# Optimization experiments

Hardware: AMD Instinct MI355X
Metric: run time of the kernel (lower is better)

The kernel has to match this reference:

```python
import jax, jax.numpy as jnp
import numpy as np

D_IN = 768
D_OUT = 768
SEQ = 4096


def setup_inputs() -> dict:
    key = jax.random.key(0)
    kx, kq, kk, kv = jax.random.split(key, 4)
    # nn.Linear weight shape is [d_out, d_in]; kaiming-uniform-ish scale
    s = 1.0 / np.sqrt(D_IN)
    return {
        "x": jax.random.normal(kx, (SEQ, D_IN), dtype=jnp.float32),
        "Wq": jax.random.uniform(kq, (D_OUT, D_IN), jnp.float32, -s, s),
        "Wk": jax.random.uniform(kk, (D_OUT, D_IN), jnp.float32, -s, s),
        "Wv": jax.random.uniform(kv, (D_OUT, D_IN), jnp.float32, -s, s),
    }


def reference(x, Wq, Wk, Wv):
    # queries/keys/values: [S, d_out] = x @ W.T
    q = x @ Wq.T
    k = x @ Wk.T
    v = x @ Wv.T
    scale = 1.0 / jnp.sqrt(jnp.asarray(k.shape[-1], x.dtype))
    scores = (q @ k.T) * scale               # [S, S]
    attn = jax.nn.softmax(scores, axis=-1)   # [S, S]
    return attn @ v                          # [S, d_out]
```

## Files before the change

### kernel.cpp

```cpp
#include <hip/hip_runtime.h>
#include <hip/hip_bf16.h>

using bf16 = __hip_bfloat16;
typedef __attribute__((ext_vector_type(4))) float f32x4;
typedef __attribute__((ext_vector_type(8))) short short8;

#define SEQ 4096
#define DIM 768


__global__ void convert_all_kernel(const float* __restrict__ x,
                                   const float* __restrict__ wq,
                                   const float* __restrict__ wk,
                                   const float* __restrict__ wv,
                                   bf16* __restrict__ xc, bf16* __restrict__ wqc,
                                   bf16* __restrict__ wkc, bf16* __restrict__ wvc,
                                   float* __restrict__ denom) {
  const int XB = (SEQ * DIM) / 2048;
  const int WB = (DIM * DIM) / 2048;
  int b = blockIdx.x;
  if (b == 0) {
    float4 z = {0.f, 0.f, 0.f, 0.f};
#pragma unroll
    for (int q = 0; q < 4; q++)
      *(float4*)(denom + (threadIdx.x * 4 + q * 1024)) = z;
  }
  const float* src; bf16* dst; int off;
  if (b < XB)               { src = x;  dst = xc;  off = b * 2048; }
  else if (b < XB + WB)     { src = wq; dst = wqc; off = (b - XB) * 2048; }
  else if (b < XB + 2 * WB) { src = wk; dst = wkc; off = (b - XB - WB) * 2048; }
  else                      { src = wv; dst = wvc; off = (b - XB - 2 * WB) * 2048; }
  int i = off + threadIdx.x * 8;
  float4 f0 = *(const float4*)(src + i);
  float4 f1 = *(const float4*)(src + i + 4);
  bf16 tmp[8];
  tmp[0] = __float2bfloat16(f0.x); tmp[1] = __float2bfloat16(f0.y);
  tmp[2] = __float2bfloat16(f0.z); tmp[3] = __float2bfloat16(f0.w);
  tmp[4] = __float2bfloat16(f1.x); tmp[5] = __float2bfloat16(f1.y);
  tmp[6] = __float2bfloat16(f1.z); tmp[7] = __float2bfloat16(f1.w);
  *(uint4*)(dst + i) = *(const uint4*)tmp;
}

__device__ __forceinline__ void gload_lds16(const bf16* g, bf16* l) {
  __builtin_amdgcn_global_load_lds(
      (const __attribute__((address_space(1))) void*)g,
      (__attribute__((address_space(3))) void*)l,
      16, 0, 0);
}

__device__ __forceinline__ void stage64(const bf16* g, int ldk, bf16* l,
                                        int wave, int lane) {
  int r = lane >> 2;
  int c = (lane & 3) * 8;
  const bf16* gw = g + (size_t)(wave * 32) * ldk;
  bf16* lw = l + wave * 1024;
#pragma unroll
  for (int h = 0; h < 2; h++)
#pragma unroll
    for (int s = 0; s < 2; s++)
      gload_lds16(gw + (size_t)(s * 16 + r) * ldk + h * 32 + c,
                  lw + h * 4096 + s * 512);
}

__device__ __forceinline__ void gemm_core(const bf16* __restrict__ A,
                                          const bf16* __restrict__ B,
                                          int ldk, int klen, int m0, int n0,
                                          f32x4 acc[4][4],
                                          bf16* lA, bf16* lB) {
  const int tid  = threadIdx.x;
  const int wave = tid >> 6, lane = tid & 63;
  const int wm = (wave & 1) * 64, wn = (wave >> 1) * 64;
  const int g = lane >> 4, lr = lane & 15;
  const bf16* Abase = A + (size_t)m0 * ldk;
  const bf16* Bbase = B + (size_t)n0 * ldk;
  for (int kk = 0; kk < klen; kk += 64) {
    stage64(Abase + kk, ldk, lA, wave, lane);
    stage64(Bbase + kk, ldk, lB, wave, lane);
    __syncthreads();
#pragma unroll
    for (int h = 0; h < 2; h++) {
      short8 af[4], bfr[4];
#pragma unroll
      for (int i = 0; i < 4; i++)
        af[i] = *(const short8*)&lA[h * 4096 + (wm + i * 16 + lr) * 32 + g * 8];
#pragma unroll
      for (int j = 0; j < 4; j++)
        bfr[j] = *(const short8*)&lB[h * 4096 + (wn + j * 16 + lr) * 32 + g * 8];
#pragma unroll
      for (int i = 0; i < 4; i++)
#pragma unroll
        for (int j = 0; j < 4; j++)
          acc[i][j] = __builtin_amdgcn_mfma_f32_16x16x32_bf16(af[i], bfr[j], acc[i][j], 0, 0, 0);
    }
    __syncthreads();
  }
}


__global__ __launch_bounds__(256, 3) void qkv_kernel(
    const bf16* __restrict__ x, const bf16* __restrict__ Wq,
    const bf16* __restrict__ Wk, const bf16* __restrict__ Wv,
    bf16* __restrict__ Q, bf16* __restrict__ Kb, bf16* __restrict__ Vt) {
  __shared__ __align__(16) bf16 smem[16384];
  bf16* lA = smem;
  bf16* lB = smem + 8192;
  const int m0  = blockIdx.x * 128;
  const int n0g = blockIdx.y * 128;
  const int wsel = n0g / DIM;
  const int n0   = n0g % DIM;
  const bf16* W = (wsel == 0) ? Wq : (wsel == 1) ? Wk : Wv;
  f32x4 acc[4][4] = {};
  gemm_core(x, W, DIM, DIM, m0, n0, acc, lA, lB);

  const int tid = threadIdx.x, wave = tid >> 6, lane = tid & 63;
  const int wm = (wave & 1) * 64, wn = (wave >> 1) * 64;
  const int g = lane >> 4, lr = lane & 15;
  const float scale = 0.03608439182435161f;

  if (wsel == 2) {
    bf16* tile = smem;
#pragma unroll
    for (int ph = 0; ph < 2; ph++) {
      __syncthreads();
      if ((wave >> 1) == ph) {
#pragma unroll
        for (int i = 0; i < 4; i++)
#pragma unroll
          for (int j = 0; j < 4; j++)
#pragma unroll
            for (int r = 0; r < 4; r++)
              tile[(wm + i * 16 + g * 4 + r) * 67 + j * 16 + lr] =
                  __float2bfloat16(acc[i][j][r]);
      }
      __syncthreads();
      int cl = tid >> 2;
      int r0 = (tid & 3) * 32;
      bf16 vals[32];
#pragma unroll
      for (int k = 0; k < 32; k++) vals[k] = tile[(r0 + k) * 67 + cl];
      bf16* dst = Vt + (size_t)(n0 + ph * 64 + cl) * SEQ + m0 + r0;
#pragma unroll
      for (int q = 0; q < 4; q++)
        *(uint4*)(dst + q * 8) = *(const uint4*)(vals + q * 8);
    }
  } else {
    bf16* dstm = (wsel == 0) ? Q : Kb;
    float fs = (wsel == 0) ? scale : 1.0f;
#pragma unroll
    for (int i = 0; i < 4; i++)
#pragma unroll
      for (int j = 0; j < 4; j++)
#pragma unroll
        for (int r = 0; r < 4; r++) {
          int row = m0 + wm + i * 16 + g * 4 + r;
          int col = n0 + wn + j * 16 + lr;
          dstm[row * DIM + col] = __float2bfloat16(acc[i][j][r] * fs);
        }
  }
}

__global__ __launch_bounds__(256, 3) void score_kernel(
    const bf16* __restrict__ Q, const bf16* __restrict__ Kb,
    bf16* __restrict__ P, float* __restrict__ denom) {
  __shared__ __align__(16) bf16 smem[16384];
  bf16* lA = smem;
  bf16* lB = smem + 8192;
  const int m0 = blockIdx.x * 128;
  const int n0 = blockIdx.y * 128;
  f32x4 acc[4][4] = {};
  gemm_core(Q, Kb, DIM, DIM, m0, n0, acc, lA, lB);

  const int tid = threadIdx.x, wave = tid >> 6, lane = tid & 63;
  const int wm = (wave & 1) * 64, wn = (wave >> 1) * 64;
  const int g = lane >> 4, lr = lane & 15;
#pragma unroll
  for (int i = 0; i < 4; i++) {
    float rsum[4] = {0.f, 0.f, 0.f, 0.f};
#pragma unroll
    for (int j = 0; j < 4; j++)
#pragma unroll
      for (int r = 0; r < 4; r++) {
        float p = __expf(acc[i][j][r]);
        int row = m0 + wm + i * 16 + g * 4 + r;
        int col = n0 + wn + j * 16 + lr;
        P[row * SEQ + col] = __float2bfloat16(p);
        rsum[r] += p;
      }
#pragma unroll
    for (int r = 0; r < 4; r++) {
      float s = rsum[r];
      s += __shfl_xor(s, 1);
      s += __shfl_xor(s, 2);
      s += __shfl_xor(s, 4);
      s += __shfl_xor(s, 8);
      if (lr == 0) atomicAdd(&denom[m0 + wm + i * 16 + g * 4 + r], s);
    }
  }
}

__global__ __launch_bounds__(256, 3) void pv_kernel(
    const bf16* __restrict__ P, const bf16* __restrict__ Vt,
    bf16* __restrict__ partial) {
  __shared__ __align__(16) bf16 smem[16384];
  bf16* lA = smem;
  bf16* lB = smem + 8192;
  const int m0 = blockIdx.x * 128;
  const int n0 = blockIdx.y * 128;
  const int kbase = blockIdx.z * (SEQ / 4);
  f32x4 acc[4][4] = {};
  gemm_core(P + kbase, Vt + kbase, SEQ, SEQ / 4, m0, n0, acc, lA, lB);

  bf16* pout = partial + (size_t)blockIdx.z * SEQ * DIM;
  const int tid = threadIdx.x, wave = tid >> 6, lane = tid & 63;
  const int wm = (wave & 1) * 64, wn = (wave >> 1) * 64;
  const int g = lane >> 4, lr = lane & 15;
#pragma unroll
  for (int i = 0; i < 4; i++)
#pragma unroll
    for (int j = 0; j < 4; j++)
#pragma unroll
      for (int r = 0; r < 4; r++) {
        int row = m0 + wm + i * 16 + g * 4 + r;
        int col = n0 + wn + j * 16 + lr;
        pout[row * DIM + col] = __float2bfloat16(acc[i][j][r]);
      }
}

__global__ __launch_bounds__(256) void reduce_kernel(
    const bf16* __restrict__ partial, const float* __restrict__ denom,
    float* __restrict__ out) {
  const size_t stride = (size_t)SEQ * DIM;
  int i = (blockIdx.x * 256 + threadIdx.x) * 8;
  uint4 u0 = *(const uint4*)(partial + i);
  uint4 u1 = *(const uint4*)(partial + stride + i);
  uint4 u2 = *(const uint4*)(partial + 2 * stride + i);
  uint4 u3 = *(const uint4*)(partial + 3 * stride + i);
  bf16 a0[8], a1[8], a2[8], a3[8];
  *(uint4*)a0 = u0; *(uint4*)a1 = u1; *(uint4*)a2 = u2; *(uint4*)a3 = u3;
  float inv = 1.0f / denom[i / DIM];
  float o[8];
#pragma unroll
  for (int k = 0; k < 8; k++)
    o[k] = (__bfloat162float(a0[k]) + __bfloat162float(a1[k]) +
            __bfloat162float(a2[k]) + __bfloat162float(a3[k])) * inv;
  *(float4*)(out + i)     = *(const float4*)(o);
  *(float4*)(out + i + 4) = *(const float4*)(o + 4);
}

extern "C" void kernel_launch(void* const* d_in, const int* in_sizes, int n_in,
                              void* d_out, int out_size, void* d_ws, size_t ws_size,
                              hipStream_t stream) {
  const float* x_raw  = (const float*)d_in[0];
  const float* Wq_raw = (const float*)d_in[1];
  const float* Wk_raw = (const float*)d_in[2];
  const float* Wv_raw = (const float*)d_in[3];
  float* out = (float*)d_out;

  bf16* xc  = (bf16*)d_ws;
  bf16* Wqc = xc  + (size_t)SEQ * DIM;
  bf16* Wkc = Wqc + (size_t)DIM * DIM;
  bf16* Wvc = Wkc + (size_t)DIM * DIM;
  bf16* Q   = Wvc + (size_t)DIM * DIM;
  bf16* Kb  = Q   + (size_t)SEQ * DIM;
  bf16* Vt  = Kb  + (size_t)SEQ * DIM;
  bf16* P   = Vt  + (size_t)DIM * SEQ;
  float* denom  = (float*)(P + (size_t)SEQ * SEQ);
  bf16* partial = (bf16*)(denom + SEQ);

  const int nx = SEQ * DIM;
  const int nw = DIM * DIM;
  const int conv_blocks = nx / 2048 + 3 * (nw / 2048);

  convert_all_kernel<<<conv_blocks, 256, 0, stream>>>(
      x_raw, Wq_raw, Wk_raw, Wv_raw, xc, Wqc, Wkc, Wvc, denom);
  qkv_kernel<<<dim3(SEQ / 128, 2304 / 128), 256, 0, stream>>>(xc, Wqc, Wkc, Wvc, Q, Kb, Vt);
  score_kernel<<<dim3(SEQ / 128, SEQ / 128), 256, 0, stream>>>(Q, Kb, P, denom);
  pv_kernel<<<dim3(SEQ / 128, DIM / 128, 4), 256, 0, stream>>>(P, Vt, partial);
  reduce_kernel<<<nx / 8 / 256, 256, 0, stream>>>(partial, denom, out);
}
```

Baseline: 167.1 us.

## Load GEMM fragments directly from global memory with padded row strides

```diff
diff --git a/kernel.cpp b/kernel.cpp
--- a/kernel.cpp
+++ b/kernel.cpp
@@ -7,6 +7,8 @@
 
 #define SEQ 4096
 #define DIM 768
+#define LDQ 800
+#define LDP 4128
 
 
 __global__ void convert_all_kernel(const float* __restrict__ x,
@@ -16,101 +18,73 @@
                                    bf16* __restrict__ xc, bf16* __restrict__ wqc,
                                    bf16* __restrict__ wkc, bf16* __restrict__ wvc,
                                    float* __restrict__ denom) {
-  const int XB = (SEQ * DIM) / 2048;
-  const int WB = (DIM * DIM) / 2048;
+  const int XB = SEQ * 96 / 256;
+  const int WB = DIM * 96 / 256;
   int b = blockIdx.x;
   if (b == 0) {
     float4 z = {0.f, 0.f, 0.f, 0.f};
 #pragma unroll
     for (int q = 0; q < 4; q++)
-      *(float4*)(denom + (threadIdx.x * 4 + q * 1024)) = z;
-  }
-  const float* src; bf16* dst; int off;
-  if (b < XB)               { src = x;  dst = xc;  off = b * 2048; }
-  else if (b < XB + WB)     { src = wq; dst = wqc; off = (b - XB) * 2048; }
-  else if (b < XB + 2 * WB) { src = wk; dst = wkc; off = (b - XB - WB) * 2048; }
-  else                      { src = wv; dst = wvc; off = (b - XB - 2 * WB) * 2048; }
-  int i = off + threadIdx.x * 8;
-  float4 f0 = *(const float4*)(src + i);
-  float4 f1 = *(const float4*)(src + i + 4);
+      *(float4*)(denom + threadIdx.x * 4 + q * 1024) = z;
+  }
+  const float* src; bf16* dst; int t;
+  if (b < XB)               { src = x;  dst = xc;  t = b * 256 + threadIdx.x; }
+  else if (b < XB + WB)     { src = wq; dst = wqc; t = (b - XB) * 256 + threadIdx.x; }
+  else if (b < XB + 2 * WB) { src = wk; dst = wkc; t = (b - XB - WB) * 256 + threadIdx.x; }
+  else                      { src = wv; dst = wvc; t = (b - XB - 2 * WB) * 256 + threadIdx.x; }
+  int row = t / 96;
+  int col = (t - row * 96) * 8;
+  const float* s = src + row * DIM + col;
+  float4 f0 = *(const float4*)s;
+  float4 f1 = *(const float4*)(s + 4);
   bf16 tmp[8];
   tmp[0] = __float2bfloat16(f0.x); tmp[1] = __float2bfloat16(f0.y);
   tmp[2] = __float2bfloat16(f0.z); tmp[3] = __float2bfloat16(f0.w);
   tmp[4] = __float2bfloat16(f1.x); tmp[5] = __float2bfloat16(f1.y);
   tmp[6] = __float2bfloat16(f1.z); tmp[7] = __float2bfloat16(f1.w);
-  *(uint4*)(dst + i) = *(const uint4*)tmp;
-}
-
-__device__ __forceinline__ void gload_lds16(const bf16* g, bf16* l) {
-  __builtin_amdgcn_global_load_lds(
-      (const __attribute__((address_space(1))) void*)g,
-      (__attribute__((address_space(3))) void*)l,
-      16, 0, 0);
-}
-
-__device__ __forceinline__ void stage64(const bf16* g, int ldk, bf16* l,
-                                        int wave, int lane) {
-  int r = lane >> 2;
-  int c = (lane & 3) * 8;
-  const bf16* gw = g + (size_t)(wave * 32) * ldk;
-  bf16* lw = l + wave * 1024;
-#pragma unroll
-  for (int h = 0; h < 2; h++)
-#pragma unroll
-    for (int s = 0; s < 2; s++)
-      gload_lds16(gw + (size_t)(s * 16 + r) * ldk + h * 32 + c,
-                  lw + h * 4096 + s * 512);
-}
-
-__device__ __forceinline__ void gemm_core(const bf16* __restrict__ A,
-                                          const bf16* __restrict__ B,
-                                          int ldk, int klen, int m0, int n0,
-                                          f32x4 acc[4][4],
-                                          bf16* lA, bf16* lB) {
-  const int tid  = threadIdx.x;
+  *(uint4*)(dst + row * LDQ + col) = *(const uint4*)tmp;
+}
+
+__device__ __forceinline__ void gemm_direct(const bf16* __restrict__ A,
+                                            const bf16* __restrict__ B,
+                                            int ldk, int klen, int m0, int n0,
+                                            f32x4 acc[4][4]) {
+  const int tid = threadIdx.x;
   const int wave = tid >> 6, lane = tid & 63;
   const int wm = (wave & 1) * 64, wn = (wave >> 1) * 64;
   const int g = lane >> 4, lr = lane & 15;
-  const bf16* Abase = A + (size_t)m0 * ldk;
-  const bf16* Bbase = B + (size_t)n0 * ldk;
-  for (int kk = 0; kk < klen; kk += 64) {
-    stage64(Abase + kk, ldk, lA, wave, lane);
-    stage64(Bbase + kk, ldk, lB, wave, lane);
-    __syncthreads();
-#pragma unroll
-    for (int h = 0; h < 2; h++) {
-      short8 af[4], bfr[4];
-#pragma unroll
-      for (int i = 0; i < 4; i++)
-        af[i] = *(const short8*)&lA[h * 4096 + (wm + i * 16 + lr) * 32 + g * 8];
+  const bf16* Ab = A + (size_t)(m0 + wm + lr) * ldk + g * 8;
+  const bf16* Bb = B + (size_t)(n0 + wn + lr) * ldk + g * 8;
+  const size_t r16 = (size_t)16 * ldk;
+  for (int kk = 0; kk < klen; kk += 32) {
+    short8 af[4], bfr[4];
+#pragma unroll
+    for (int i = 0; i < 4; i++)
+      af[i] = *(const short8*)(Ab + i * r16 + kk);
+#pragma unroll
+    for (int j = 0; j < 4; j++)
+      bfr[j] = *(const short8*)(Bb + j * r16 + kk);
+#pragma unroll
+    for (int i = 0; i < 4; i++)
 #pragma unroll
       for (int j = 0; j < 4; j++)
-        bfr[j] = *(const short8*)&lB[h * 4096 + (wn + j * 16 + lr) * 32 + g * 8];
-#pragma unroll
-      for (int i = 0; i < 4; i++)
-#pragma unroll
-        for (int j = 0; j < 4; j++)
-          acc[i][j] = __builtin_amdgcn_mfma_f32_16x16x32_bf16(af[i], bfr[j], acc[i][j], 0, 0, 0);
-    }
-    __syncthreads();
-  }
-}
-
-
-__global__ __launch_bounds__(256, 3) void qkv_kernel(
+        acc[i][j] = __builtin_amdgcn_mfma_f32_16x16x32_bf16(af[i], bfr[j], acc[i][j], 0, 0, 0);
+  }
+}
+
+
+__global__ __launch_bounds__(256, 4) void qkv_kernel(
     const bf16* __restrict__ x, const bf16* __restrict__ Wq,
     const bf16* __restrict__ Wk, const bf16* __restrict__ Wv,
     bf16* __restrict__ Q, bf16* __restrict__ Kb, bf16* __restrict__ Vt) {
-  __shared__ __align__(16) bf16 smem[16384];
-  bf16* lA = smem;
-  bf16* lB = smem + 8192;
+  __shared__ __align__(16) bf16 tile[128 * 67];
   const int m0  = blockIdx.x * 128;
   const int n0g = blockIdx.y * 128;
   const int wsel = n0g / DIM;
   const int n0   = n0g % DIM;
   const bf16* W = (wsel == 0) ? Wq : (wsel == 1) ? Wk : Wv;
   f32x4 acc[4][4] = {};
-  gemm_core(x, W, DIM, DIM, m0, n0, acc, lA, lB);
+  gemm_direct(x, W, LDQ, DIM, m0, n0, acc);
 
   const int tid = threadIdx.x, wave = tid >> 6, lane = tid & 63;
   const int wm = (wave & 1) * 64, wn = (wave >> 1) * 64;
@@ -118,7 +92,6 @@
   const float scale = 0.03608439182435161f;
 
   if (wsel == 2) {
-    bf16* tile = smem;
 #pragma unroll
     for (int ph = 0; ph < 2; ph++) {
       __syncthreads();
@@ -138,7 +111,7 @@
       bf16 vals[32];
 #pragma unroll
       for (int k = 0; k < 32; k++) vals[k] = tile[(r0 + k) * 67 + cl];
-      bf16* dst = Vt + (size_t)(n0 + ph * 64 + cl) * SEQ + m0 + r0;
+      bf16* dst = Vt + (size_t)(n0 + ph * 64 + cl) * LDP + m0 + r0;
 #pragma unroll
       for (int q = 0; q < 4; q++)
         *(uint4*)(dst + q * 8) = *(const uint4*)(vals + q * 8);
@@ -154,21 +127,18 @@
         for (int r = 0; r < 4; r++) {
           int row = m0 + wm + i * 16 + g * 4 + r;
           int col = n0 + wn + j * 16 + lr;
-          dstm[row * DIM + col] = __float2bfloat16(acc[i][j][r] * fs);
+          dstm[row * LDQ + col] = __float2bfloat16(acc[i][j][r] * fs);
         }
   }
 }
 
-__global__ __launch_bounds__(256, 3) void score_kernel(
+__global__ __launch_bounds__(256, 4) void score_kernel(
     const bf16* __restrict__ Q, const bf16* __restrict__ Kb,
     bf16* __restrict__ P, float* __restrict__ denom) {
-  __shared__ __align__(16) bf16 smem[16384];
-  bf16* lA = smem;
-  bf16* lB = smem + 8192;
   const int m0 = blockIdx.x * 128;
   const int n0 = blockIdx.y * 128;
   f32x4 acc[4][4] = {};
-  gemm_core(Q, Kb, DIM, DIM, m0, n0, acc, lA, lB);
+  gemm_direct(Q, Kb, LDQ, DIM, m0, n0, acc);
 
   const int tid = threadIdx.x, wave = tid >> 6, lane = tid & 63;
   const int wm = (wave & 1) * 64, wn = (wave >> 1) * 64;
@@ -183,7 +153,7 @@
         float p = __expf(acc[i][j][r]);
         int row = m0 + wm + i * 16 + g * 4 + r;
         int col = n0 + wn + j * 16 + lr;
-        P[row * SEQ + col] = __float2bfloat16(p);
+        P[(size_t)row * LDP + col] = __float2bfloat16(p);
         rsum[r] += p;
       }
 #pragma unroll
@@ -198,17 +168,14 @@
   }
 }
 
-__global__ __launch_bounds__(256, 3) void pv_kernel(
+__global__ __launch_bounds__(256, 4) void pv_kernel(
     const bf16* __restrict__ P, const bf16* __restrict__ Vt,
     bf16* __restrict__ partial) {
-  __shared__ __align__(16) bf16 smem[16384];
-  bf16* lA = smem;
-  bf16* lB = smem + 8192;
   const int m0 = blockIdx.x * 128;
   const int n0 = blockIdx.y * 128;
   const int kbase = blockIdx.z * (SEQ / 4);
   f32x4 acc[4][4] = {};
-  gemm_core(P + kbase, Vt + kbase, SEQ, SEQ / 4, m0, n0, acc, lA, lB);
+  gemm_direct(P + kbase, Vt + kbase, LDP, SEQ / 4, m0, n0, acc);
 
   bf16* pout = partial + (size_t)blockIdx.z * SEQ * DIM;
   const int tid = threadIdx.x, wave = tid >> 6, lane = tid & 63;
@@ -257,24 +224,22 @@
   float* out = (float*)d_out;
 
   bf16* xc  = (bf16*)d_ws;
-  bf16* Wqc = xc  + (size_t)SEQ * DIM;
-  bf16* Wkc = Wqc + (size_t)DIM * DIM;
-  bf16* Wvc = Wkc + (size_t)DIM * DIM;
-  bf16* Q   = Wvc + (size_t)DIM * DIM;
-  bf16* Kb  = Q   + (size_t)SEQ * DIM;
-  bf16* Vt  = Kb  + (size_t)SEQ * DIM;
-  bf16* P   = Vt  + (size_t)DIM * SEQ;
-  float* denom  = (float*)(P + (size_t)SEQ * SEQ);
+  bf16* Wqc = xc  + (size_t)SEQ * LDQ;
+  bf16* Wkc = Wqc + (size_t)DIM * LDQ;
+  bf16* Wvc = Wkc + (size_t)DIM * LDQ;
+  bf16* Q   = Wvc + (size_t)DIM * LDQ;
+  bf16* Kb  = Q   + (size_t)SEQ * LDQ;
+  bf16* Vt  = Kb  + (size_t)SEQ * LDQ;
+  bf16* P   = Vt  + (size_t)DIM * LDP;
+  float* denom  = (float*)(P + (size_t)SEQ * LDP);
   bf16* partial = (bf16*)(denom + SEQ);
 
-  const int nx = SEQ * DIM;
-  const int nw = DIM * DIM;
-  const int conv_blocks = nx / 2048 + 3 * (nw / 2048);
+  const int conv_blocks = SEQ * 96 / 256 + 3 * (DIM * 96 / 256);
 
   convert_all_kernel<<<conv_blocks, 256, 0, stream>>>(
       x_raw, Wq_raw, Wk_raw, Wv_raw, xc, Wqc, Wkc, Wvc, denom);
   qkv_kernel<<<dim3(SEQ / 128, 2304 / 128), 256, 0, stream>>>(xc, Wqc, Wkc, Wvc, Q, Kb, Vt);
   score_kernel<<<dim3(SEQ / 128, SEQ / 128), 256, 0, stream>>>(Q, Kb, P, denom);
   pv_kernel<<<dim3(SEQ / 128, DIM / 128, 4), 256, 0, stream>>>(P, Vt, partial);
-  reduce_kernel<<<nx / 8 / 256, 256, 0, stream>>>(partial, denom, out);
-}
+  reduce_kernel<<<SEQ * DIM / 8 / 256, 256, 0, stream>>>(partial, denom, out);
+}
```

Measured after the change: 251.6 us. 50.5% more time.

## Fuse split-K reduction and normalization into PV kernel via atomic adds

Applied to the files above, without the earlier changes.

```diff
diff --git a/kernel.cpp b/kernel.cpp
--- a/kernel.cpp
+++ b/kernel.cpp
@@ -15,7 +15,8 @@
                                    const float* __restrict__ wv,
                                    bf16* __restrict__ xc, bf16* __restrict__ wqc,
                                    bf16* __restrict__ wkc, bf16* __restrict__ wvc,
-                                   float* __restrict__ denom) {
+                                   float* __restrict__ denom,
+                                   float* __restrict__ out) {
   const int XB = (SEQ * DIM) / 2048;
   const int WB = (DIM * DIM) / 2048;
   int b = blockIdx.x;
@@ -23,10 +24,15 @@
     float4 z = {0.f, 0.f, 0.f, 0.f};
 #pragma unroll
     for (int q = 0; q < 4; q++)
-      *(float4*)(denom + (threadIdx.x * 4 + q * 1024)) = z;
+      *(float4*)(denom + threadIdx.x * 4 + q * 1024) = z;
   }
   const float* src; bf16* dst; int off;
-  if (b < XB)               { src = x;  dst = xc;  off = b * 2048; }
+  if (b < XB) {
+    src = x; dst = xc; off = b * 2048;
+    float4 z = {0.f, 0.f, 0.f, 0.f};
+    float* o = out + off + threadIdx.x * 8;
+    *(float4*)o = z; *(float4*)(o + 4) = z;
+  }
   else if (b < XB + WB)     { src = wq; dst = wqc; off = (b - XB) * 2048; }
   else if (b < XB + 2 * WB) { src = wk; dst = wkc; off = (b - XB - WB) * 2048; }
   else                      { src = wv; dst = wvc; off = (b - XB - 2 * WB) * 2048; }
@@ -183,7 +189,7 @@
         float p = __expf(acc[i][j][r]);
         int row = m0 + wm + i * 16 + g * 4 + r;
         int col = n0 + wn + j * 16 + lr;
-        P[row * SEQ + col] = __float2bfloat16(p);
+        P[(size_t)row * SEQ + col] = __float2bfloat16(p);
         rsum[r] += p;
       }
 #pragma unroll
@@ -200,7 +206,7 @@
 
 __global__ __launch_bounds__(256, 3) void pv_kernel(
     const bf16* __restrict__ P, const bf16* __restrict__ Vt,
-    bf16* __restrict__ partial) {
+    const float* __restrict__ denom, float* __restrict__ out) {
   __shared__ __align__(16) bf16 smem[16384];
   bf16* lA = smem;
   bf16* lB = smem + 8192;
@@ -210,41 +216,24 @@
   f32x4 acc[4][4] = {};
   gemm_core(P + kbase, Vt + kbase, SEQ, SEQ / 4, m0, n0, acc, lA, lB);
 
-  bf16* pout = partial + (size_t)blockIdx.z * SEQ * DIM;
   const int tid = threadIdx.x, wave = tid >> 6, lane = tid & 63;
   const int wm = (wave & 1) * 64, wn = (wave >> 1) * 64;
   const int g = lane >> 4, lr = lane & 15;
 #pragma unroll
-  for (int i = 0; i < 4; i++)
+  for (int i = 0; i < 4; i++) {
+    float inv[4];
+#pragma unroll
+    for (int r = 0; r < 4; r++)
+      inv[r] = 1.0f / denom[m0 + wm + i * 16 + g * 4 + r];
 #pragma unroll
     for (int j = 0; j < 4; j++)
 #pragma unroll
       for (int r = 0; r < 4; r++) {
         int row = m0 + wm + i * 16 + g * 4 + r;
         int col = n0 + wn + j * 16 + lr;
-        pout[row * DIM + col] = __float2bfloat16(acc[i][j][r]);
+        atomicAdd(&out[row * DIM + col], acc[i][j][r] * inv[r]);
       }
-}
-
-__global__ __launch_bounds__(256) void reduce_kernel(
-    const bf16* __restrict__ partial, const float* __restrict__ denom,
-    float* __restrict__ out) {
-  const size_t stride = (size_t)SEQ * DIM;
-  int i = (blockIdx.x * 256 + threadIdx.x) * 8;
-  uint4 u0 = *(const uint4*)(partial + i);
-  uint4 u1 = *(const uint4*)(partial + stride + i);
-  uint4 u2 = *(const uint4*)(partial + 2 * stride + i);
-  uint4 u3 = *(const uint4*)(partial + 3 * stride + i);
-  bf16 a0[8], a1[8], a2[8], a3[8];
-  *(uint4*)a0 = u0; *(uint4*)a1 = u1; *(uint4*)a2 = u2; *(uint4*)a3 = u3;
-  float inv = 1.0f / denom[i / DIM];
-  float o[8];
-#pragma unroll
-  for (int k = 0; k < 8; k++)
-    o[k] = (__bfloat162float(a0[k]) + __bfloat162float(a1[k]) +
-            __bfloat162float(a2[k]) + __bfloat162float(a3[k])) * inv;
-  *(float4*)(out + i)     = *(const float4*)(o);
-  *(float4*)(out + i + 4) = *(const float4*)(o + 4);
+  }
 }
 
 extern "C" void kernel_launch(void* const* d_in, const int* in_sizes, int n_in,
@@ -264,17 +253,15 @@
   bf16* Kb  = Q   + (size_t)SEQ * DIM;
   bf16* Vt  = Kb  + (size_t)SEQ * DIM;
   bf16* P   = Vt  + (size_t)DIM * SEQ;
-  float* denom  = (float*)(P + (size_t)SEQ * SEQ);
-  bf16* partial = (bf16*)(denom + SEQ);
+  float* denom = (float*)(P + (size_t)SEQ * SEQ);
 
   const int nx = SEQ * DIM;
   const int nw = DIM * DIM;
   const int conv_blocks = nx / 2048 + 3 * (nw / 2048);
 
   convert_all_kernel<<<conv_blocks, 256, 0, stream>>>(
-      x_raw, Wq_raw, Wk_raw, Wv_raw, xc, Wqc, Wkc, Wvc, denom);
+      x_raw, Wq_raw, Wk_raw, Wv_raw, xc, Wqc, Wkc, Wvc, denom, out);
   qkv_kernel<<<dim3(SEQ / 128, 2304 / 128), 256, 0, stream>>>(xc, Wqc, Wkc, Wvc, Q, Kb, Vt);
   score_kernel<<<dim3(SEQ / 128, SEQ / 128), 256, 0, stream>>>(Q, Kb, P, denom);
-  pv_kernel<<<dim3(SEQ / 128, DIM / 128, 4), 256, 0, stream>>>(P, Vt, partial);
-  reduce_kernel<<<nx / 8 / 256, 256, 0, stream>>>(partial, denom, out);
-}
+  pv_kernel<<<dim3(SEQ / 128, DIM / 128, 4), 256, 0, stream>>>(P, Vt, denom, out);
+}
```

Measured after the change: 192.3 us. +15.0%, slower.
